# Optimization experiments

Measured on AMD Instinct MI355X. Metric: run time of the kernel, lower is better.

The kernel has to match this reference:

```python
import jax, jax.numpy as jnp
import numpy as np

N = 4096
INPUT_DIM = 256
HIDDEN = 64
HEADS = 8
NEG_SLOPE = 0.2
MASK_FILL = -10000.0


def setup_inputs() -> dict:
    key = jax.random.key(0)
    k_x, k_adj, k_w, k_as, k_ad = jax.random.split(key, 5)
    x = jax.random.normal(k_x, (N, INPUT_DIM), dtype=jnp.float32)
    adjacency = jax.random.bernoulli(k_adj, 0.05, (N, N)) | jnp.eye(N, dtype=bool)
    # linear weight, torch convention: [out_features, in_features]
    W = jax.random.normal(k_w, (HEADS * HIDDEN, INPUT_DIM), dtype=jnp.float32) * 0.05
    attn_src = jax.random.normal(k_as, (HEADS, HIDDEN), dtype=jnp.float32) * 0.1
    attn_dst = jax.random.normal(k_ad, (HEADS, HIDDEN), dtype=jnp.float32) * 0.1
    return {"x": x, "adjacency": adjacency, "W": W, "attn_src": attn_src, "attn_dst": attn_dst}


def reference(x, adjacency, W, attn_src, attn_dst):
    # h: [N, heads, hidden]
    h = (x @ W.T).reshape(N, HEADS, HIDDEN)
    src_scores = jnp.einsum('nhd,hd->nh', h, attn_src)  # [N, heads]
    dst_scores = jnp.einsum('nhd,hd->nh', h, attn_dst)  # [N, heads]
    # logits[i, j, h] = src[i, h] + dst[j, h]  (matches torch permute(2,0,1) layout math)
    logits = src_scores[:, None, :] + dst_scores[None, :, :]  # [N, N, heads]
    logits = jax.nn.leaky_relu(logits, negative_slope=NEG_SLOPE)
    logits = jnp.where(adjacency[:, :, None], logits, MASK_FILL)
    alpha = jax.nn.softmax(logits, axis=1)  # softmax over source nodes j
    out = jnp.einsum('ijh,jhf->ihf', alpha, h)  # [N, heads, hidden]
    return out.mean(axis=1)  # [N, hidden]
```

## Files before the change

kernel.cpp:

```cpp
#include <hip/hip_runtime.h>

#define NN 4096
#define IN_DIM 256
#define HID 64
#define HEADS 8

typedef __attribute__((ext_vector_type(4))) float f32x4;
typedef __attribute__((ext_vector_type(8))) short s16x8;
typedef unsigned short u16;
typedef unsigned long long u64;

__device__ inline u16 f2bf(float f) {
  union { float f; unsigned u; } v; v.f = f;
  unsigned r = (v.u + 0x7FFFu + ((v.u >> 16) & 1u)) >> 16;
  return (u16)r;
}
__device__ inline float bf2f(u16 b) {
  union { unsigned u; float f; } v; v.u = ((unsigned)b) << 16;
  return v.f;
}
__device__ __forceinline__ unsigned cvt_pk_bf16(float a, float b) {
  unsigned r;
  asm("v_cvt_pk_bf16_f32 %0, %1, %2" : "=v"(r) : "v"(a), "v"(b));
  return r;
}
__device__ inline unsigned encf(float f) {
  unsigned u = __float_as_uint(f);
  return (u & 0x80000000u) ? ~u : (u | 0x80000000u);
}
__device__ inline float decf(unsigned k) {
  return (k & 0x80000000u) ? __uint_as_float(k & 0x7FFFFFFFu) : __uint_as_float(~k);
}

__global__ __launch_bounds__(256) void gat_pack(
    const void* __restrict__ adj, u64* __restrict__ bits)
{
  __shared__ int smode;
  const int t = threadIdx.x;
  if (t < 64) {
    const unsigned char* a8 = (const unsigned char*)adj;
    const int* a32 = (const int*)adj;
    size_t i8 = (size_t)(4 * t + 1) * 4097;
    int p8 = a8[i8] != 0;
    size_t k = (size_t)(2 * t + 1);
    int p32 = a32[k * 4097] != 0;
    int p64 = a32[2 * k * 4097] != 0;
    int ok8 = __all(p8), ok32 = __all(p32), ok64 = __all(p64);
    if (t == 0) smode = ok8 ? 0 : (ok32 ? 1 : (ok64 ? 2 : 1));
  }
  __syncthreads();
  const int mode = smode;

  const int lane = t & 63;
  const int wave = (blockIdx.x * blockDim.x + t) >> 6;
  const int nwaves = (gridDim.x * blockDim.x) >> 6;
  const size_t nwords = (size_t)NN * NN / 64;

  for (size_t w = wave; w < nwords; w += nwaves) {
    size_t e = w * 64 + lane;
    int on;
    if (mode == 1)      on = ((const int*)adj)[e] != 0;
    else if (mode == 0) on = ((const unsigned char*)adj)[e] != 0;
    else                on = ((const long long*)adj)[e] != 0;
    u64 b = __ballot(on);
    if (lane == 0) bits[w] = b;
  }
}

__global__ __launch_bounds__(256) void gat_gemm1(
    const float* __restrict__ x, const float* __restrict__ W,
    const float* __restrict__ a_src, const float* __restrict__ a_dst,
    u16* __restrict__ Hbt, float* __restrict__ s_srcT,
    float* __restrict__ s_dstT, unsigned* __restrict__ Mh_enc)
{
  __shared__ u16 xhi[64 * 72], xlo[64 * 72], whi[64 * 72], wlo[64 * 72];
  const int nb = blockIdx.x;
  const int ob = blockIdx.y;
  const int t = threadIdx.x;
  const int lane = t & 63, wid = t >> 6;
  const int wr = wid >> 1, wc = wid & 1;
  const int g = lane >> 4;

  f32x4 acc[2][2] = {};

  const int sn = t >> 2;
  const int skc = (t & 3) * 16;

  for (int kb = 0; kb < 4; ++kb) {
    const float* xr = x + (size_t)(nb * 64 + sn) * IN_DIM + kb * 64 + skc;
    const float* wr_p = W + (size_t)(ob * 64 + sn) * IN_DIM + kb * 64 + skc;
#pragma unroll
    for (int c = 0; c < 4; ++c) {
      float4 xv = ((const float4*)xr)[c];
      float4 wv = ((const float4*)wr_p)[c];
      float xf[4] = {xv.x, xv.y, xv.z, xv.w};
      float wf[4] = {wv.x, wv.y, wv.z, wv.w};
      u16 xh[4], xl[4], wh[4], wl[4];
#pragma unroll
      for (int e = 0; e < 4; ++e) {
        xh[e] = f2bf(xf[e]); xl[e] = f2bf(xf[e] - bf2f(xh[e]));
        wh[e] = f2bf(wf[e]); wl[e] = f2bf(wf[e] - bf2f(wh[e]));
      }
      int base = sn * 72 + skc + c * 4;
      *(ushort4*)(xhi + base) = make_ushort4(xh[0], xh[1], xh[2], xh[3]);
      *(ushort4*)(xlo + base) = make_ushort4(xl[0], xl[1], xl[2], xl[3]);
      *(ushort4*)(whi + base) = make_ushort4(wh[0], wh[1], wh[2], wh[3]);
      *(ushort4*)(wlo + base) = make_ushort4(wl[0], wl[1], wl[2], wl[3]);
    }
    __syncthreads();
#pragma unroll
    for (int ks = 0; ks < 2; ++ks) {
      const int k0 = ks * 32 + g * 8;
      s16x8 ah[2], al[2], bh[2], bl[2];
#pragma unroll
      for (int nf = 0; nf < 2; ++nf) {
        int row = wr * 32 + nf * 16 + (lane & 15);
        ah[nf] = *(const s16x8*)(xhi + row * 72 + k0);
        al[nf] = *(const s16x8*)(xlo + row * 72 + k0);
      }
#pragma unroll
      for (int of = 0; of < 2; ++of) {
        int row = wc * 32 + of * 16 + (lane & 15);
        bh[of] = *(const s16x8*)(whi + row * 72 + k0);
        bl[of] = *(const s16x8*)(wlo + row * 72 + k0);
      }
#pragma unroll
      for (int nf = 0; nf < 2; ++nf)
#pragma unroll
        for (int of = 0; of < 2; ++of) {
          acc[nf][of] = __builtin_amdgcn_mfma_f32_16x16x32_bf16(ah[nf], bh[of], acc[nf][of], 0, 0, 0);
          acc[nf][of] = __builtin_amdgcn_mfma_f32_16x16x32_bf16(ah[nf], bl[of], acc[nf][of], 0, 0, 0);
          acc[nf][of] = __builtin_amdgcn_mfma_f32_16x16x32_bf16(al[nf], bh[of], acc[nf][of], 0, 0, 0);
        }
    }
    __syncthreads();
  }

  u16* Ct = xhi;
#pragma unroll
  for (int nf = 0; nf < 2; ++nf)
#pragma unroll
    for (int of = 0; of < 2; ++of)
#pragma unroll
      for (int r = 0; r < 4; ++r) {
        int nloc = wr * 32 + nf * 16 + g * 4 + r;
        int oloc = wc * 32 + of * 16 + (lane & 15);
        Ct[oloc * 72 + nloc] = f2bf(acc[nf][of][r]);
      }

  {
    const float* asp = a_src + ob * 64;
    const float* adp = a_dst + ob * 64;
    float as0 = asp[wc * 32 + (lane & 15)], as1 = asp[wc * 32 + 16 + (lane & 15)];
    float ad0 = adp[wc * 32 + (lane & 15)], ad1 = adp[wc * 32 + 16 + (lane & 15)];
    float* sred = (float*)wlo;
#pragma unroll
    for (int nf = 0; nf < 2; ++nf)
#pragma unroll
      for (int r = 0; r < 4; ++r) {
        float vs = acc[nf][0][r] * as0 + acc[nf][1][r] * as1;
        float vd = acc[nf][0][r] * ad0 + acc[nf][1][r] * ad1;
#pragma unroll
        for (int m = 1; m < 16; m <<= 1) { vs += __shfl_xor(vs, m); vd += __shfl_xor(vd, m); }
        if ((lane & 15) == 0) {
          int node = wr * 32 + nf * 16 + g * 4 + r;
          sred[wc * 64 + node] = vs;
          sred[128 + wc * 64 + node] = vd;
        }
      }
  }
  __syncthreads();
  {
    int o = t >> 2, nc = (t & 3) * 16;
    u16* dst = Hbt + ((size_t)(ob * 64 + nb) * 64 + o) * 64 + nc;
#pragma unroll
    for (int c = 0; c < 2; ++c) {
      s16x8 v = *(const s16x8*)(Ct + o * 72 + nc + c * 8);
      *(s16x8*)(dst + c * 8) = v;
    }
  }
  if (t < 64) {
    const float* sred = (const float*)wlo;
    float vssum = sred[t] + sred[64 + t];
    float vdsum = sred[128 + t] + sred[192 + t];
    s_srcT[(size_t)ob * NN + nb * 64 + t] = vssum;
    s_dstT[(size_t)ob * NN + nb * 64 + t] = vdsum;
    float m = vdsum;
#pragma unroll
    for (int s = 1; s < 64; s <<= 1) m = fmaxf(m, __shfl_xor(m, s));
    if (t == 0) atomicMax(Mh_enc + ob, encf(m));
  }
}

__global__ __launch_bounds__(512, 4) void gat_flash(
    const u64* __restrict__ bits, const u16* __restrict__ Hbt,
    const float* __restrict__ s_srcT, const float* __restrict__ s_dstT,
    const unsigned* __restrict__ Mh_enc, float* __restrict__ pout)
{
  __shared__ char shmem[32768];
  __shared__ float Lbuf[8][16];
  u16* Ast = (u16*)shmem;

  const int t = threadIdx.x, lane = t & 63, wid = t >> 6;
  const int ws4 = wid & 3, jh = wid >> 2;
  const int bid = blockIdx.x;
  const int h = bid & 7, iblk = bid >> 3;
  const int i_loc = lane & 15, g = lane >> 4, j0 = g * 8;
  const int irow = iblk * 64 + ws4 * 16 + i_loc;

  const float s_i = s_srcT[(size_t)h * NN + irow];
  float m_i = s_i + decf(Mh_enc[h]);
  m_i = fmaxf(m_i, 0.2f * m_i);
  const float L2E = 1.44269504f;
  const float mL = m_i * L2E;

  const u16* tile0 = Hbt + (size_t)h * 64 * 4096;
  const float* dT = s_dstT + (size_t)h * NN;

  const int lt = t & 255;
  const int r0 = lt >> 3, colE = (lt & 7) * 8;
  const int jtb = jh * 32;
  const u16* gsrc0 = tile0 + (size_t)jtb * 4096 + r0 * 64 + (colE ^ ((r0 & 7) << 3));
  const u16* gsrc1 = tile0 + (size_t)jtb * 4096 + (32 + r0) * 64 + (colE ^ ((r0 & 7) << 3));
  const u64* brow = bits + (size_t)irow * 64 + jtb;
  const float* dp = dT + jtb * 64 + j0;

  u16* sdstA = Ast + jh * 8192;
  u16* sdstB = sdstA + 4096;
  const char* lbaseA = (const char*)sdstA;
  const char* lbaseB = (const char*)sdstB;
  const int swz = (i_loc & 7) << 4;
  const int ofA0 = (g * 16) ^ swz, ofA1 = ((g * 16) + 64) ^ swz;

  s16x8 ones;
#pragma unroll
  for (int e = 0; e < 8; ++e) ones[e] = (short)0x3F80;

  f32x4 acc[4] = {};
  f32x4 acc_l = {0.f, 0.f, 0.f, 0.f};

#define QUAD(DV, MBITS, SH, PW0, PW1) do {                            \
    float z0 = s_i + DV[0], z1 = s_i + DV[1];                         \
    float z2 = s_i + DV[2], z3 = s_i + DV[3];                         \
    z0 = fmaxf(z0, 0.2f * z0); z1 = fmaxf(z1, 0.2f * z1);             \
    z2 = fmaxf(z2, 0.2f * z2); z3 = fmaxf(z3, 0.2f * z3);             \
    float e0 = __builtin_amdgcn_exp2f(__builtin_fmaf(z0, L2E, -mL));  \
    float e1 = __builtin_amdgcn_exp2f(__builtin_fmaf(z1, L2E, -mL));  \
    float e2 = __builtin_amdgcn_exp2f(__builtin_fmaf(z2, L2E, -mL));  \
    float e3 = __builtin_amdgcn_exp2f(__builtin_fmaf(z3, L2E, -mL));  \
    e0 = ((MBITS >> (SH + 0)) & 1u) ? e0 : 0.f;                       \
    e1 = ((MBITS >> (SH + 1)) & 1u) ? e1 : 0.f;                       \
    e2 = ((MBITS >> (SH + 2)) & 1u) ? e2 : 0.f;                       \
    e3 = ((MBITS >> (SH + 3)) & 1u) ? e3 : 0.f;                       \
    PW0 = cvt_pk_bf16(e0, e1); PW1 = cvt_pk_bf16(e2, e3);             \
  } while (0)

#define TILE_BODY(SDST, LBASE) do {                                   \
    *(s16x8*)((SDST) + lt * 8) = sv0;                                 \
    *(s16x8*)((SDST) + 2048 + lt * 8) = sv1;                          \
    gsrc0 += 4096; gsrc1 += 4096;                                     \
    sv0 = *(const s16x8*)(gsrc0);                                     \
    sv1 = *(const s16x8*)(gsrc1);                                     \
    const u64 am_ = *brow++;                                          \
    f32x4 d0 = *(const f32x4*)(dp);                                   \
    f32x4 d1 = *(const f32x4*)(dp + 4);                               \
    f32x4 d2 = *(const f32x4*)(dp + 32);                              \
    f32x4 d3 = *(const f32x4*)(dp + 36);                              \
    dp += 64;                                                         \
    const unsigned amlo = (unsigned)(am_ >> j0);                      \
    const unsigned amhi = (unsigned)(am_ >> (32 + j0));               \
    union { unsigned w_[4]; s16x8 v_; } P0, P1;                       \
    QUAD(d0, amlo, 0, P0.w_[0], P0.w_[1]);                            \
    QUAD(d1, amlo, 4, P0.w_[2], P0.w_[3]);                            \
    QUAD(d2, amhi, 0, P1.w_[0], P1.w_[1]);                            \
    QUAD(d3, amhi, 4, P1.w_[2], P1.w_[3]);                            \
    __syncthreads();                                                  \
    _Pragma("unroll")                                                 \
    for (int fb = 0; fb < 4; ++fb) {                                  \
      const int rowb = (fb * 16 + i_loc) * 128;                       \
      s16x8 A0 = *(const s16x8*)((LBASE) + rowb + ofA0);              \
      s16x8 A1 = *(const s16x8*)((LBASE) + rowb + ofA1);              \
      acc[fb] = __builtin_amdgcn_mfma_f32_16x16x32_bf16(A0, P0.v_, acc[fb], 0, 0, 0); \
      acc[fb] = __builtin_amdgcn_mfma_f32_16x16x32_bf16(A1, P1.v_, acc[fb], 0, 0, 0); \
    }                                                                 \
    acc_l = __builtin_amdgcn_mfma_f32_16x16x32_bf16(ones, P0.v_, acc_l, 0, 0, 0); \
    acc_l = __builtin_amdgcn_mfma_f32_16x16x32_bf16(ones, P1.v_, acc_l, 0, 0, 0); \
  } while (0)

  s16x8 sv0 = *(const s16x8*)(gsrc0);
  s16x8 sv1 = *(const s16x8*)(gsrc1);

  for (int it = 0; it < 16; ++it) {
    TILE_BODY(sdstA, lbaseA);
    TILE_BODY(sdstB, lbaseB);
  }
#undef QUAD
#undef TILE_BODY

  float l_run = acc_l[0];
  if (lane < 16) Lbuf[wid][i_loc] = l_run;

  __syncthreads();
  float* accst = (float*)shmem;
  if (jh == 1) {
    float* ab = accst + (ws4 * 16 + i_loc) * 66;
#pragma unroll
    for (int fb = 0; fb < 4; ++fb)
      *(f32x4*)(ab + fb * 16 + g * 4) = acc[fb];
  }
  __syncthreads();
  if (jh == 0) {
    const float invL = 1.f / (l_run + Lbuf[4 + ws4][i_loc]);
    float* ob = pout + ((size_t)h * NN + irow) * 64;
#pragma unroll
    for (int fb = 0; fb < 4; ++fb) {
      f32x4 v = acc[fb] +
          *(const f32x4*)(accst + (ws4 * 16 + i_loc) * 66 + fb * 16 + g * 4);
      *(f32x4*)(ob + fb * 16 + g * 4) = v * invL;
    }
  }
}

__global__ __launch_bounds__(256) void gat_combine(
    const float* __restrict__ pout, float* __restrict__ out)
{
  size_t e = (size_t)blockIdx.x * 256 + threadIdx.x;
  f32x4 s = {0.f, 0.f, 0.f, 0.f};
#pragma unroll
  for (int h = 0; h < 8; ++h)
    s += ((const f32x4*)pout)[(size_t)h * (NN * 16) + e];
  ((f32x4*)out)[e] = s * 0.125f;
}

extern "C" void kernel_launch(void* const* d_in, const int* in_sizes, int n_in,
                              void* d_out, int out_size, void* d_ws, size_t ws_size,
                              hipStream_t stream)
{
  const float* x = (const float*)d_in[0];
  const void* adj = d_in[1];
  const float* W = (const float*)d_in[2];
  const float* a_src = (const float*)d_in[3];
  const float* a_dst = (const float*)d_in[4];
  float* out = (float*)d_out;

  char* ws = (char*)d_ws;
  float* pout = (float*)ws;
  u16* Hbt = (u16*)(ws + 8 * 1024 * 1024);
  float* s_srcT = (float*)(ws + 12 * 1024 * 1024);
  float* s_dstT = (float*)(ws + 12 * 1024 * 1024 + 128 * 1024);
  unsigned* Mh_enc = (unsigned*)(ws + 12 * 1024 * 1024 + 384 * 1024);
  u64* bits = (u64*)(ws + 12 * 1024 * 1024 + 512 * 1024);

  hipMemsetAsync(Mh_enc, 0, 32, stream);
  gat_pack<<<2048, 256, 0, stream>>>(adj, bits);
  gat_gemm1<<<dim3(64, 8), 256, 0, stream>>>(x, W, a_src, a_dst, Hbt,
                                             s_srcT, s_dstT, Mh_enc);
  gat_flash<<<512, 512, 0, stream>>>(bits, Hbt, s_srcT, s_dstT, Mh_enc, pout);
  gat_combine<<<256, 256, 0, stream>>>(pout, out);
}
```

Before: 98.50 us.

## Split flash attention over source-node halves to double grid size

Templates the flash kernel on a J-split factor so each block handles half the source columns, launching 1024 blocks instead of 512. Unnormalized partial accumulators and partial softmax denominators are written to workspace, and a new combine kernel sums both halves and normalizes before averaging heads. This aims to fill more CUs on the MI355X (512 blocks is low for 256 CUs at 4 blocks/CU), at the cost of twice the partial-output traffic and a workspace-size-dependent fallback path.

```diff
diff --git a/kernel.cpp b/kernel.cpp
--- a/kernel.cpp
+++ b/kernel.cpp
@@ -192,19 +192,23 @@
   }
 }
 
+template <int JSPLIT>
 __global__ __launch_bounds__(512, 4) void gat_flash(
     const u64* __restrict__ bits, const u16* __restrict__ Hbt,
     const float* __restrict__ s_srcT, const float* __restrict__ s_dstT,
-    const unsigned* __restrict__ Mh_enc, float* __restrict__ pout)
+    const unsigned* __restrict__ Mh_enc, float* __restrict__ pout,
+    float* __restrict__ lpart)
 {
   __shared__ char shmem[32768];
   __shared__ float Lbuf[8][16];
   u16* Ast = (u16*)shmem;
 
   const int t = threadIdx.x, lane = t & 63, wid = t >> 6;
-  const int ws4 = wid & 3, jh = wid >> 2;
+  const int ws4 = wid & 3, jq = wid >> 2;
   const int bid = blockIdx.x;
-  const int h = bid & 7, iblk = bid >> 3;
+  const int h = bid & 7;
+  const int jhalf = (JSPLIT == 1) ? 0 : ((bid >> 3) & 1);
+  const int iblk = (JSPLIT == 1) ? (bid >> 3) : (bid >> 4);
   const int i_loc = lane & 15, g = lane >> 4, j0 = g * 8;
   const int irow = iblk * 64 + ws4 * 16 + i_loc;
 
@@ -217,15 +221,16 @@
   const u16* tile0 = Hbt + (size_t)h * 64 * 4096;
   const float* dT = s_dstT + (size_t)h * NN;
 
+  const int NT = 32 / JSPLIT;
   const int lt = t & 255;
   const int r0 = lt >> 3, colE = (lt & 7) * 8;
-  const int jtb = jh * 32;
+  const int jtb = jhalf * 32 + jq * NT;
   const u16* gsrc0 = tile0 + (size_t)jtb * 4096 + r0 * 64 + (colE ^ ((r0 & 7) << 3));
   const u16* gsrc1 = tile0 + (size_t)jtb * 4096 + (32 + r0) * 64 + (colE ^ ((r0 & 7) << 3));
   const u64* brow = bits + (size_t)irow * 64 + jtb;
   const float* dp = dT + jtb * 64 + j0;
 
-  u16* sdstA = Ast + jh * 8192;
+  u16* sdstA = Ast + jq * 8192;
   u16* sdstB = sdstA + 4096;
   const char* lbaseA = (const char*)sdstA;
   const char* lbaseB = (const char*)sdstB;
@@ -290,7 +295,7 @@
   s16x8 sv0 = *(const s16x8*)(gsrc0);
   s16x8 sv1 = *(const s16x8*)(gsrc1);
 
-  for (int it = 0; it < 16; ++it) {
+  for (int it = 0; it < NT / 2; ++it) {
     TILE_BODY(sdstA, lbaseA);
     TILE_BODY(sdstB, lbaseB);
   }
@@ -302,26 +307,37 @@
 
   __syncthreads();
   float* accst = (float*)shmem;
-  if (jh == 1) {
+  if (jq == 1) {
     float* ab = accst + (ws4 * 16 + i_loc) * 66;
 #pragma unroll
     for (int fb = 0; fb < 4; ++fb)
       *(f32x4*)(ab + fb * 16 + g * 4) = acc[fb];
   }
   __syncthreads();
-  if (jh == 0) {
-    const float invL = 1.f / (l_run + Lbuf[4 + ws4][i_loc]);
-    float* ob = pout + ((size_t)h * NN + irow) * 64;
-#pragma unroll
-    for (int fb = 0; fb < 4; ++fb) {
-      f32x4 v = acc[fb] +
-          *(const f32x4*)(accst + (ws4 * 16 + i_loc) * 66 + fb * 16 + g * 4);
-      *(f32x4*)(ob + fb * 16 + g * 4) = v * invL;
+  if (jq == 0) {
+    const float ltot = l_run + Lbuf[4 + ws4][i_loc];
+    float* ob = pout + ((size_t)(jhalf * 8 + h) * NN + irow) * 64;
+    if (JSPLIT == 1) {
+      const float invL = 1.f / ltot;
+#pragma unroll
+      for (int fb = 0; fb < 4; ++fb) {
+        f32x4 v = acc[fb] +
+            *(const f32x4*)(accst + (ws4 * 16 + i_loc) * 66 + fb * 16 + g * 4);
+        *(f32x4*)(ob + fb * 16 + g * 4) = v * invL;
+      }
+    } else {
+      if (lane < 16) lpart[(size_t)(jhalf * 8 + h) * NN + irow] = ltot;
+#pragma unroll
+      for (int fb = 0; fb < 4; ++fb) {
+        f32x4 v = acc[fb] +
+            *(const f32x4*)(accst + (ws4 * 16 + i_loc) * 66 + fb * 16 + g * 4);
+        *(f32x4*)(ob + fb * 16 + g * 4) = v;
+      }
     }
   }
 }
 
-__global__ __launch_bounds__(256) void gat_combine(
+__global__ __launch_bounds__(256) void gat_combine1(
     const float* __restrict__ pout, float* __restrict__ out)
 {
   size_t e = (size_t)blockIdx.x * 256 + threadIdx.x;
@@ -329,6 +345,23 @@
 #pragma unroll
   for (int h = 0; h < 8; ++h)
     s += ((const f32x4*)pout)[(size_t)h * (NN * 16) + e];
+  ((f32x4*)out)[e] = s * 0.125f;
+}
+
+__global__ __launch_bounds__(256) void gat_combine2(
+    const float* __restrict__ pout, const float* __restrict__ lpart,
+    float* __restrict__ out)
+{
+  size_t e = (size_t)blockIdx.x * 256 + threadIdx.x;
+  int i = (int)(e >> 4);
+  const f32x4* p4 = (const f32x4*)pout;
+  f32x4 s = {0.f, 0.f, 0.f, 0.f};
+#pragma unroll
+  for (int h = 0; h < 8; ++h) {
+    f32x4 a = p4[(size_t)h * (NN * 16) + e] + p4[(size_t)(8 + h) * (NN * 16) + e];
+    float l = lpart[(size_t)h * NN + i] + lpart[(size_t)(8 + h) * NN + i];
+    s += a * (1.f / l);
+  }
   ((f32x4*)out)[e] = s * 0.125f;
 }
 
@@ -344,17 +377,38 @@
   float* out = (float*)d_out;
 
   char* ws = (char*)d_ws;
-  float* pout = (float*)ws;
-  u16* Hbt = (u16*)(ws + 8 * 1024 * 1024);
-  float* s_srcT = (float*)(ws + 12 * 1024 * 1024);
-  float* s_dstT = (float*)(ws + 12 * 1024 * 1024 + 128 * 1024);
-  unsigned* Mh_enc = (unsigned*)(ws + 12 * 1024 * 1024 + 384 * 1024);
-  u64* bits = (u64*)(ws + 12 * 1024 * 1024 + 512 * 1024);
-
-  hipMemsetAsync(Mh_enc, 0, 32, stream);
-  gat_pack<<<2048, 256, 0, stream>>>(adj, bits);
-  gat_gemm1<<<dim3(64, 8), 256, 0, stream>>>(x, W, a_src, a_dst, Hbt,
-                                             s_srcT, s_dstT, Mh_enc);
-  gat_flash<<<512, 512, 0, stream>>>(bits, Hbt, s_srcT, s_dstT, Mh_enc, pout);
-  gat_combine<<<256, 256, 0, stream>>>(pout, out);
-}
+  const bool big = ws_size >= (size_t)24 * 1024 * 1024;
+
+  if (big) {
+    float* pout = (float*)ws;
+    u16* Hbt = (u16*)(ws + 16 * 1024 * 1024);
+    float* s_srcT = (float*)(ws + 20 * 1024 * 1024);
+    float* s_dstT = (float*)(ws + 20 * 1024 * 1024 + 128 * 1024);
+    unsigned* Mh_enc = (unsigned*)(ws + 20 * 1024 * 1024 + 384 * 1024);
+    float* lpart = (float*)(ws + 20 * 1024 * 1024 + 512 * 1024);
+    u64* bits = (u64*)(ws + 21 * 1024 * 1024);
+
+    hipMemsetAsync(Mh_enc, 0, 32, stream);
+    gat_pack<<<2048, 256, 0, stream>>>(adj, bits);
+    gat_gemm1<<<dim3(64, 8), 256, 0, stream>>>(x, W, a_src, a_dst, Hbt,
+                                               s_srcT, s_dstT, Mh_enc);
+    gat_flash<2><<<1024, 512, 0, stream>>>(bits, Hbt, s_srcT, s_dstT, Mh_enc,
+                                           pout, lpart);
+    gat_combine2<<<256, 256, 0, stream>>>(pout, lpart, out);
+  } else {
+    float* pout = (float*)ws;
+    u16* Hbt = (u16*)(ws + 8 * 1024 * 1024);
+    float* s_srcT = (float*)(ws + 12 * 1024 * 1024);
+    float* s_dstT = (float*)(ws + 12 * 1024 * 1024 + 128 * 1024);
+    unsigned* Mh_enc = (unsigned*)(ws + 12 * 1024 * 1024 + 384 * 1024);
+    u64* bits = (u64*)(ws + 12 * 1024 * 1024 + 512 * 1024);
+
+    hipMemsetAsync(Mh_enc, 0, 32, stream);
+    gat_pack<<<2048, 256, 0, stream>>>(adj, bits);
+    gat_gemm1<<<dim3(64, 8), 256, 0, stream>>>(x, W, a_src, a_dst, Hbt,
+                                               s_srcT, s_dstT, Mh_enc);
+    gat_flash<1><<<512, 512, 0, stream>>>(bits, Hbt, s_srcT, s_dstT, Mh_enc,
+                                          pout, nullptr);
+    gat_combine1<<<256, 256, 0, stream>>>(pout, out);
+  }
+}
```

New measurement: 102.3 us. 3.8% more time.

## Factor leaky-ReLU softmax exponentials into per-node precomputed terms

Applied to the files above, without the earlier changes.

Splits exp(leaky(s_i+d_j)-m_i) into a per-row factor times a per-column factor, exp(d_j) or exp(0.2 d_j). The branch is chosen by comparing exp(d_j) against exp(-s_i). The column factors are computed once in the projection kernel, which removes every per-element exp2 from the flash loop's inner body. In exchange, two float arrays are loaded per tile instead of one. The factorised form can overflow or underflow in fp32 for large scores, and the workspace offsets are reshuffled.

```diff
diff --git a/kernel.cpp b/kernel.cpp
--- a/kernel.cpp
+++ b/kernel.cpp
@@ -71,7 +71,8 @@
     const float* __restrict__ x, const float* __restrict__ W,
     const float* __restrict__ a_src, const float* __restrict__ a_dst,
     u16* __restrict__ Hbt, float* __restrict__ s_srcT,
-    float* __restrict__ s_dstT, unsigned* __restrict__ Mh_enc)
+    float* __restrict__ F1, float* __restrict__ F2,
+    unsigned* __restrict__ Mh_enc)
 {
   __shared__ u16 xhi[64 * 72], xlo[64 * 72], whi[64 * 72], wlo[64 * 72];
   const int nb = blockIdx.x;
@@ -183,8 +184,10 @@
     const float* sred = (const float*)wlo;
     float vssum = sred[t] + sred[64 + t];
     float vdsum = sred[128 + t] + sred[192 + t];
+    const float L2E = 1.44269504f;
     s_srcT[(size_t)ob * NN + nb * 64 + t] = vssum;
-    s_dstT[(size_t)ob * NN + nb * 64 + t] = vdsum;
+    F1[(size_t)ob * NN + nb * 64 + t] = __builtin_amdgcn_exp2f(vdsum * L2E);
+    F2[(size_t)ob * NN + nb * 64 + t] = __builtin_amdgcn_exp2f(0.2f * vdsum * L2E);
     float m = vdsum;
 #pragma unroll
     for (int s = 1; s < 64; s <<= 1) m = fmaxf(m, __shfl_xor(m, s));
@@ -194,8 +197,9 @@
 
 __global__ __launch_bounds__(512, 4) void gat_flash(
     const u64* __restrict__ bits, const u16* __restrict__ Hbt,
-    const float* __restrict__ s_srcT, const float* __restrict__ s_dstT,
-    const unsigned* __restrict__ Mh_enc, float* __restrict__ pout)
+    const float* __restrict__ s_srcT, const float* __restrict__ F1,
+    const float* __restrict__ F2, const unsigned* __restrict__ Mh_enc,
+    float* __restrict__ pout)
 {
   __shared__ char shmem[32768];
   __shared__ float Lbuf[8][16];
@@ -208,14 +212,16 @@
   const int i_loc = lane & 15, g = lane >> 4, j0 = g * 8;
   const int irow = iblk * 64 + ws4 * 16 + i_loc;
 
+  const float L2E = 1.44269504f;
   const float s_i = s_srcT[(size_t)h * NN + irow];
   float m_i = s_i + decf(Mh_enc[h]);
   m_i = fmaxf(m_i, 0.2f * m_i);
-  const float L2E = 1.44269504f;
   const float mL = m_i * L2E;
+  const float a1 = __builtin_amdgcn_exp2f(__builtin_fmaf(s_i, L2E, -mL));
+  const float a2 = __builtin_amdgcn_exp2f(__builtin_fmaf(0.2f * s_i, L2E, -mL));
+  const float th = __builtin_amdgcn_exp2f(-s_i * L2E);
 
   const u16* tile0 = Hbt + (size_t)h * 64 * 4096;
-  const float* dT = s_dstT + (size_t)h * NN;
 
   const int lt = t & 255;
   const int r0 = lt >> 3, colE = (lt & 7) * 8;
@@ -223,7 +229,8 @@
   const u16* gsrc0 = tile0 + (size_t)jtb * 4096 + r0 * 64 + (colE ^ ((r0 & 7) << 3));
   const u16* gsrc1 = tile0 + (size_t)jtb * 4096 + (32 + r0) * 64 + (colE ^ ((r0 & 7) << 3));
   const u64* brow = bits + (size_t)irow * 64 + jtb;
-  const float* dp = dT + jtb * 64 + j0;
+  const float* p1 = F1 + (size_t)h * NN + jtb * 64 + j0;
+  const float* p2 = F2 + (size_t)h * NN + jtb * 64 + j0;
 
   u16* sdstA = Ast + jh * 8192;
   u16* sdstB = sdstA + 4096;
@@ -239,15 +246,13 @@
   f32x4 acc[4] = {};
   f32x4 acc_l = {0.f, 0.f, 0.f, 0.f};
 
-#define QUAD(DV, MBITS, SH, PW0, PW1) do {                            \
-    float z0 = s_i + DV[0], z1 = s_i + DV[1];                         \
-    float z2 = s_i + DV[2], z3 = s_i + DV[3];                         \
-    z0 = fmaxf(z0, 0.2f * z0); z1 = fmaxf(z1, 0.2f * z1);             \
-    z2 = fmaxf(z2, 0.2f * z2); z3 = fmaxf(z3, 0.2f * z3);             \
-    float e0 = __builtin_amdgcn_exp2f(__builtin_fmaf(z0, L2E, -mL));  \
-    float e1 = __builtin_amdgcn_exp2f(__builtin_fmaf(z1, L2E, -mL));  \
-    float e2 = __builtin_amdgcn_exp2f(__builtin_fmaf(z2, L2E, -mL));  \
-    float e3 = __builtin_amdgcn_exp2f(__builtin_fmaf(z3, L2E, -mL));  \
+#define QUAD(V1, V2, MBITS, SH, PW0, PW1) do {                        \
+    bool c0 = V1[0] > th, c1 = V1[1] > th;                            \
+    bool c2 = V1[2] > th, c3 = V1[3] > th;                            \
+    float e0 = (c0 ? a1 : a2) * (c0 ? V1[0] : V2[0]);                 \
+    float e1 = (c1 ? a1 : a2) * (c1 ? V1[1] : V2[1]);                 \
+    float e2 = (c2 ? a1 : a2) * (c2 ? V1[2] : V2[2]);                 \
+    float e3 = (c3 ? a1 : a2) * (c3 ? V1[3] : V2[3]);                 \
     e0 = ((MBITS >> (SH + 0)) & 1u) ? e0 : 0.f;                       \
     e1 = ((MBITS >> (SH + 1)) & 1u) ? e1 : 0.f;                       \
     e2 = ((MBITS >> (SH + 2)) & 1u) ? e2 : 0.f;                       \
@@ -262,18 +267,22 @@
     sv0 = *(const s16x8*)(gsrc0);                                     \
     sv1 = *(const s16x8*)(gsrc1);                                     \
     const u64 am_ = *brow++;                                          \
-    f32x4 d0 = *(const f32x4*)(dp);                                   \
-    f32x4 d1 = *(const f32x4*)(dp + 4);                               \
-    f32x4 d2 = *(const f32x4*)(dp + 32);                              \
-    f32x4 d3 = *(const f32x4*)(dp + 36);                              \
-    dp += 64;                                                         \
+    f32x4 v1a = *(const f32x4*)(p1);                                  \
+    f32x4 v1b = *(const f32x4*)(p1 + 4);                              \
+    f32x4 v1c = *(const f32x4*)(p1 + 32);                             \
+    f32x4 v1d = *(const f32x4*)(p1 + 36);                             \
+    f32x4 v2a = *(const f32x4*)(p2);                                  \
+    f32x4 v2b = *(const f32x4*)(p2 + 4);                              \
+    f32x4 v2c = *(const f32x4*)(p2 + 32);                             \
+    f32x4 v2d = *(const f32x4*)(p2 + 36);                             \
+    p1 += 64; p2 += 64;                                               \
     const unsigned amlo = (unsigned)(am_ >> j0);                      \
     const unsigned amhi = (unsigned)(am_ >> (32 + j0));               \
     union { unsigned w_[4]; s16x8 v_; } P0, P1;                       \
-    QUAD(d0, amlo, 0, P0.w_[0], P0.w_[1]);                            \
-    QUAD(d1, amlo, 4, P0.w_[2], P0.w_[3]);                            \
-    QUAD(d2, amhi, 0, P1.w_[0], P1.w_[1]);                            \
-    QUAD(d3, amhi, 4, P1.w_[2], P1.w_[3]);                            \
+    QUAD(v1a, v2a, amlo, 0, P0.w_[0], P0.w_[1]);                      \
+    QUAD(v1b, v2b, amlo, 4, P0.w_[2], P0.w_[3]);                      \
+    QUAD(v1c, v2c, amhi, 0, P1.w_[0], P1.w_[1]);                      \
+    QUAD(v1d, v2d, amhi, 4, P1.w_[2], P1.w_[3]);                      \
     __syncthreads();                                                  \
     _Pragma("unroll")                                                 \
     for (int fb = 0; fb < 4; ++fb) {                                  \
@@ -347,14 +356,15 @@
   float* pout = (float*)ws;
   u16* Hbt = (u16*)(ws + 8 * 1024 * 1024);
   float* s_srcT = (float*)(ws + 12 * 1024 * 1024);
-  float* s_dstT = (float*)(ws + 12 * 1024 * 1024 + 128 * 1024);
-  unsigned* Mh_enc = (unsigned*)(ws + 12 * 1024 * 1024 + 384 * 1024);
+  float* F1 = (float*)(ws + 12 * 1024 * 1024 + 128 * 1024);
+  float* F2 = (float*)(ws + 12 * 1024 * 1024 + 256 * 1024);
+  unsigned* Mh_enc = (unsigned*)(ws + 12 * 1024 * 1024 + 400 * 1024);
   u64* bits = (u64*)(ws + 12 * 1024 * 1024 + 512 * 1024);
 
   hipMemsetAsync(Mh_enc, 0, 32, stream);
   gat_pack<<<2048, 256, 0, stream>>>(adj, bits);
   gat_gemm1<<<dim3(64, 8), 256, 0, stream>>>(x, W, a_src, a_dst, Hbt,
-                                             s_srcT, s_dstT, Mh_enc);
-  gat_flash<<<512, 512, 0, stream>>>(bits, Hbt, s_srcT, s_dstT, Mh_enc, pout);
+                                             s_srcT, F1, F2, Mh_enc);
+  gat_flash<<<512, 512, 0, stream>>>(bits, Hbt, s_srcT, F1, F2, Mh_enc, pout);
   gat_combine<<<256, 256, 0, stream>>>(pout, out);
 }
```

Measured after the change: 108.3 us. 10.0% more time.
